# Kernel optimization log

Measured on AMD Instinct MI355X. Metric: run time of the kernel, lower is better.

## Reference

```python
import jax, jax.numpy as jnp
import numpy as np

B, Q, K, D, U = 8, 128, 512, 256, 256  # batch, q_len, kv_len, feat dim, units
NEG_INF = -1e6


def setup_inputs() -> dict:
    key = jax.random.key(0)
    ks = jax.random.split(key, 7)
    query = jax.random.normal(ks[0], (B, Q, D), dtype=jnp.float32)
    k_in = jax.random.normal(ks[1], (B, K, D), dtype=jnp.float32)
    value = jax.random.normal(ks[2], (B, K, D), dtype=jnp.float32)
    valid_len = jax.random.randint(ks[3], (B,), 1, K + 1, dtype=jnp.int32)
    s = 1.0 / np.sqrt(D)
    Wq = jax.random.uniform(ks[4], (D, U), jnp.float32, -s, s)
    Wk = jax.random.uniform(ks[5], (D, U), jnp.float32, -s, s)
    v_w = jax.random.uniform(ks[6], (U,), jnp.float32, -1.0 / np.sqrt(U), 1.0 / np.sqrt(U))
    return {"query": query, "key": k_in, "value": value, "valid_len": valid_len,
            "Wq": Wq, "Wk": Wk, "v_w": v_w}


def reference(query, key, value, valid_len, Wq, Wk, v_w):
    # projections: [B,Q,U] and [B,K,U]
    q = jnp.einsum('bqd,du->bqu', query, Wq)
    k = jnp.einsum('bkd,du->bku', key, Wk)
    # additive features [B,Q,K,U] -> tanh -> reduce with v: scores [B,Q,K]
    feats = jnp.tanh(q[:, :, None, :] + k[:, None, :, :])
    scores = jnp.einsum('bqku,u->bqk', feats, v_w)
    # masked softmax over keys: positions >= valid_len[b] masked out
    mask = jnp.arange(K)[None, None, :] < valid_len[:, None, None]
    scores = jnp.where(mask, scores, NEG_INF)
    attn = jax.nn.softmax(scores, axis=-1)
    # dropout p=0.0 (eval) -> identity
    return jnp.einsum('bqk,bkd->bqd', attn, value)
```

## Files before the change

### kernel.cpp

```cpp
#include <hip/hip_runtime.h>
#include <hip/hip_bf16.h>

#ifndef __has_builtin
#define __has_builtin(x) 0
#endif

__device__ __forceinline__ float fast_exp2(float x) {
#if __has_builtin(__builtin_amdgcn_exp2f)
  return __builtin_amdgcn_exp2f(x);
#else
  return exp2f(x);
#endif
}
__device__ __forceinline__ float fast_rcp(float x) {
#if __has_builtin(__builtin_amdgcn_rcpf)
  return __builtin_amdgcn_rcpf(x);
#else
  return 1.0f / x;
#endif
}

constexpr int Bsz = 8, QL = 128, KL = 512, DD = 256, UU = 256;
constexpr int PR = 4;
constexpr int DT = 8;
constexpr float NEG_INF = -1e6f;
constexpr float C2 = 2.885390081777927f;

__global__ __launch_bounds__(256) void proj_kernel(
    const float* __restrict__ query, const float* __restrict__ key,
    const float* __restrict__ Wq, const float* __restrict__ Wk,
    const int* __restrict__ valid_len,
    float* __restrict__ qp, float* __restrict__ kpT)
{
  const int u   = threadIdx.x;
  const int blk = blockIdx.x;

  constexpr int QBLKS = Bsz * QL / PR;
  const bool isQ = blk < QBLKS;
  const int  m0  = isQ ? blk * PR : (blk - QBLKS) * PR;

  const int kb_b = m0 / KL, kb_k0 = m0 % KL;
  if (!isQ) {
    if (kb_k0 >= valid_len[kb_b]) return;
  }
  const float* __restrict__ in = isQ ? query : key;
  const float* __restrict__ W  = isQ ? Wq : Wk;
  const float* r0 = in + (size_t)m0 * DD;

  float acc[PR];
#pragma unroll
  for (int r = 0; r < PR; ++r) acc[r] = 0.f;

  float  w_c[DT], w_n[DT];
  float4 r_c[PR][2], r_n[PR][2];

#pragma unroll
  for (int j = 0; j < DT; ++j) w_c[j] = W[j * UU + u];
#pragma unroll
  for (int r = 0; r < PR; ++r) {
    r_c[r][0] = *reinterpret_cast<const float4*>(r0 + r * DD);
    r_c[r][1] = *reinterpret_cast<const float4*>(r0 + r * DD + 4);
  }

  for (int d = 0; d < DD; d += DT) {
    const int dn = (d + DT < DD) ? d + DT : 0;
#pragma unroll
    for (int j = 0; j < DT; ++j) w_n[j] = W[(dn + j) * UU + u];
#pragma unroll
    for (int r = 0; r < PR; ++r) {
      r_n[r][0] = *reinterpret_cast<const float4*>(r0 + r * DD + dn);
      r_n[r][1] = *reinterpret_cast<const float4*>(r0 + r * DD + dn + 4);
    }
#pragma unroll
    for (int r = 0; r < PR; ++r) {
      float a = acc[r];
      a = fmaf(r_c[r][0].x, w_c[0], a);
      a = fmaf(r_c[r][0].y, w_c[1], a);
      a = fmaf(r_c[r][0].z, w_c[2], a);
      a = fmaf(r_c[r][0].w, w_c[3], a);
      a = fmaf(r_c[r][1].x, w_c[4], a);
      a = fmaf(r_c[r][1].y, w_c[5], a);
      a = fmaf(r_c[r][1].z, w_c[6], a);
      a = fmaf(r_c[r][1].w, w_c[7], a);
      acc[r] = a;
    }
#pragma unroll
    for (int j = 0; j < DT; ++j) w_c[j] = w_n[j];
#pragma unroll
    for (int r = 0; r < PR; ++r) { r_c[r][0] = r_n[r][0]; r_c[r][1] = r_n[r][1]; }
  }

  if (isQ) {
    float* o = qp + (size_t)m0 * UU + u;
#pragma unroll
    for (int r = 0; r < PR; ++r) o[(size_t)r * UU] = fast_exp2(acc[r] * C2);
  } else {
    float4 cv;
    cv.x = fast_exp2(acc[0] * C2); cv.y = fast_exp2(acc[1] * C2);
    cv.z = fast_exp2(acc[2] * C2); cv.w = fast_exp2(acc[3] * C2);
    *reinterpret_cast<float4*>(kpT + ((size_t)kb_b * UU + u) * KL + kb_k0) = cv;
  }
}

__global__ __launch_bounds__(512) void fused_attn_kernel(
    const float* __restrict__ value, const int* __restrict__ valid_len,
    const float* __restrict__ v_w, const float* __restrict__ qp,
    const float* __restrict__ kpT, float* __restrict__ out)
{
  __shared__ __align__(16) float4 qpack[UU];
  __shared__ __align__(16) float2 sp_part[8][8][64];
  __shared__ __align__(16) float  sps0[KL];
  __shared__ __align__(16) float  sps1[KL];
  __shared__ __align__(16) float2 opart[DD];
  __shared__ float2 redM[8], redS[8];

  const int t = threadIdx.x;
  const int w = t >> 6, l = t & 63;

  const int g = blockIdx.x;
  const int x = g & 7;
  const int i = g >> 3;
  int vl[8];
#pragma unroll
  for (int bi = 0; bi < 8; ++bi) vl[bi] = valid_len[bi];
  const int rk = (i < 32) ? x : (7 - x);
  int b = 0;
#pragma unroll
  for (int bi = 0; bi < 8; ++bi) {
    int r = 0;
#pragma unroll
    for (int bj = 0; bj < 8; ++bj)
      r += (vl[bj] > vl[bi]) || (vl[bj] == vl[bi] && bj < bi);
    if (r == rk) b = bi;
  }
  const int vlen = vl[b];
  const int q0 = i * 2;
  const int nc = (vlen + 63) >> 6;

  if (t < UU) {
    qpack[t] = make_float4(qp[(size_t)(b * QL + q0) * UU + t],
                           qp[(size_t)(b * QL + q0 + 1) * UU + t],
                           v_w[t], 0.f);
  }
  __syncthreads();

  {
    const float* __restrict__ kbase =
        kpT + ((size_t)(b * UU) + 32 * w) * KL + l;
    for (int c = 0; c < nc; ++c) {
      const int k64 = 64 * c;
      float a0 = 0.f, a1 = 0.f;
      float cb[8], nb[8];
#pragma unroll
      for (int j = 0; j < 8; ++j) cb[j] = kbase[(size_t)j * KL + k64];
#pragma unroll 1
      for (int ug = 0; ug < 32; ug += 8) {
        const int un = (ug + 8 < 32) ? ug + 8 : 0;
#pragma unroll
        for (int j = 0; j < 8; ++j) nb[j] = kbase[(size_t)(un + j) * KL + k64];
#pragma unroll
        for (int j = 0; j < 8; ++j) {
          const float4 qv = qpack[32 * w + ug + j];
          const float d0 = fmaf(qv.x, cb[j], 1.0f);
          const float d1 = fmaf(qv.y, cb[j], 1.0f);
          a0 = fmaf(qv.z, fast_rcp(d0), a0);
          a1 = fmaf(qv.z, fast_rcp(d1), a1);
        }
#pragma unroll
        for (int j = 0; j < 8; ++j) cb[j] = nb[j];
      }
      sp_part[w][c][l] = make_float2(a0, a1);
    }
  }
  __syncthreads();

  float s0 = 0.f, s1 = 0.f;
#pragma unroll
  for (int ws = 0; ws < 8; ++ws) {
    const float2 p = sp_part[ws][w][l];
    s0 += p.x; s1 += p.y;
  }
  const int key = t;
  s0 = (key < vlen) ? -(s0 + s0) : NEG_INF;
  s1 = (key < vlen) ? -(s1 + s1) : NEG_INF;

  float mx0 = s0, mx1 = s1;
#pragma unroll
  for (int off = 32; off >= 1; off >>= 1) {
    mx0 = fmaxf(mx0, __shfl_xor(mx0, off, 64));
    mx1 = fmaxf(mx1, __shfl_xor(mx1, off, 64));
  }
  if (l == 0) redM[w] = make_float2(mx0, mx1);
  __syncthreads();
  float m0 = redM[0].x, m1 = redM[0].y;
#pragma unroll
  for (int j = 1; j < 8; ++j) {
    m0 = fmaxf(m0, redM[j].x);
    m1 = fmaxf(m1, redM[j].y);
  }

  const float e0 = __expf(s0 - m0);
  const float e1 = __expf(s1 - m1);
  sps0[key] = e0;
  sps1[key] = e1;
  float ss0 = e0, ss1 = e1;
#pragma unroll
  for (int off = 32; off >= 1; off >>= 1) {
    ss0 += __shfl_xor(ss0, off, 64);
    ss1 += __shfl_xor(ss1, off, 64);
  }
  if (l == 0) redS[w] = make_float2(ss0, ss1);
  __syncthreads();
  float sum0 = redS[0].x, sum1 = redS[0].y;
#pragma unroll
  for (int j = 1; j < 8; ++j) {
    sum0 += redS[j].x;
    sum1 += redS[j].y;
  }
  const float inv0 = fast_rcp(sum0);
  const float inv1 = fast_rcp(sum1);

  const int h = t >> 8, d = t & 255;
  const int kmax  = (vlen + 15) & ~15;
  const int khalf = ((kmax >> 1) + 15) & ~15;
  const int kst = h ? khalf : 0;
  const int ken = h ? kmax : khalf;

  float o0 = 0.f, o1 = 0.f;
  if (ken > kst) {
    const float* __restrict__ vb = value + (size_t)b * KL * DD + d;
    float vc[16], vn[16];
#pragma unroll
    for (int j = 0; j < 16; ++j) vc[j] = vb[(size_t)(kst + j) * DD];
#pragma unroll 1
    for (int k = kst; k < ken; k += 16) {
      const int kn = (k + 16 < ken) ? k + 16 : kst;
#pragma unroll
      for (int j = 0; j < 16; ++j) vn[j] = vb[(size_t)(kn + j) * DD];
      const float4* __restrict__ p4 = reinterpret_cast<const float4*>(sps0 + k);
      const float4* __restrict__ q4 = reinterpret_cast<const float4*>(sps1 + k);
      const float4 p0 = p4[0], p1 = p4[1], p2 = p4[2], p3 = p4[3];
      const float4 r0 = q4[0], r1 = q4[1], r2 = q4[2], r3 = q4[3];
      o0 = fmaf(p0.x, vc[0],  o0); o1 = fmaf(r0.x, vc[0],  o1);
      o0 = fmaf(p0.y, vc[1],  o0); o1 = fmaf(r0.y, vc[1],  o1);
      o0 = fmaf(p0.z, vc[2],  o0); o1 = fmaf(r0.z, vc[2],  o1);
      o0 = fmaf(p0.w, vc[3],  o0); o1 = fmaf(r0.w, vc[3],  o1);
      o0 = fmaf(p1.x, vc[4],  o0); o1 = fmaf(r1.x, vc[4],  o1);
      o0 = fmaf(p1.y, vc[5],  o0); o1 = fmaf(r1.y, vc[5],  o1);
      o0 = fmaf(p1.z, vc[6],  o0); o1 = fmaf(r1.z, vc[6],  o1);
      o0 = fmaf(p1.w, vc[7],  o0); o1 = fmaf(r1.w, vc[7],  o1);
      o0 = fmaf(p2.x, vc[8],  o0); o1 = fmaf(r2.x, vc[8],  o1);
      o0 = fmaf(p2.y, vc[9],  o0); o1 = fmaf(r2.y, vc[9],  o1);
      o0 = fmaf(p2.z, vc[10], o0); o1 = fmaf(r2.z, vc[10], o1);
      o0 = fmaf(p2.w, vc[11], o0); o1 = fmaf(r2.w, vc[11], o1);
      o0 = fmaf(p3.x, vc[12], o0); o1 = fmaf(r3.x, vc[12], o1);
      o0 = fmaf(p3.y, vc[13], o0); o1 = fmaf(r3.y, vc[13], o1);
      o0 = fmaf(p3.z, vc[14], o0); o1 = fmaf(r3.z, vc[14], o1);
      o0 = fmaf(p3.w, vc[15], o0); o1 = fmaf(r3.w, vc[15], o1);
#pragma unroll
      for (int j = 0; j < 16; ++j) vc[j] = vn[j];
    }
  }
  if (h) opart[d] = make_float2(o0, o1);
  __syncthreads();
  if (!h) {
    const float2 p = opart[d];
    out[(size_t)(b * QL + q0) * DD + d]     = (o0 + p.x) * inv0;
    out[(size_t)(b * QL + q0 + 1) * DD + d] = (o1 + p.y) * inv1;
  }
}

extern "C" void kernel_launch(void* const* d_in, const int* in_sizes, int n_in,
                              void* d_out, int out_size, void* d_ws, size_t ws_size,
                              hipStream_t stream) {
  const float* query     = (const float*)d_in[0];
  const float* key       = (const float*)d_in[1];
  const float* value     = (const float*)d_in[2];
  const int*   valid_len = (const int*)d_in[3];
  const float* Wq        = (const float*)d_in[4];
  const float* Wk        = (const float*)d_in[5];
  const float* v_w       = (const float*)d_in[6];
  float* out = (float*)d_out;

  float* qp  = (float*)d_ws;
  float* kpT = qp + (size_t)Bsz * QL * UU;

  const int proj_blocks = (Bsz * QL + Bsz * KL) / PR;
  proj_kernel<<<proj_blocks, 256, 0, stream>>>(query, key, Wq, Wk, valid_len,
                                               qp, kpT);

  const int fused_blocks = Bsz * QL / 2;
  fused_attn_kernel<<<fused_blocks, 512, 0, stream>>>(value, valid_len, v_w,
                                                      qp, kpT, out);
}
```

Before: 113.3 us.

## Tile projection GEMM with shared-memory input rows and 8-row register blocking

The projection kernel now stages a 16-row input tile in shared memory and has each thread compute 8 rows for one of 128 output units, with two unit-halves per row tile. Each weight value loaded from global memory is reused across 8 rows instead of 4, which cuts redundant weight reads. Input rows are read from LDS as broadcasts instead of per-thread global loads. In exchange, the grid has fewer blocks, each carries a 16 KB LDS tile, and the loop is longer per thread. Masked key tiles are still skipped, but now at 16-row granularity.

```diff
diff --git a/kernel.cpp b/kernel.cpp
--- a/kernel.cpp
+++ b/kernel.cpp
@@ -21,10 +21,13 @@
 }
 
 constexpr int Bsz = 8, QL = 128, KL = 512, DD = 256, UU = 256;
-constexpr int PR = 4;
-constexpr int DT = 8;
 constexpr float NEG_INF = -1e6f;
 constexpr float C2 = 2.885390081777927f;
+
+constexpr int TR = 16;
+constexpr int TU = 128;
+constexpr int QTILES = (Bsz * QL / TR) * 2;
+constexpr int KTILES = (Bsz * KL / TR) * 2;
 
 __global__ __launch_bounds__(256) void proj_kernel(
     const float* __restrict__ query, const float* __restrict__ key,
@@ -32,73 +35,97 @@
     const int* __restrict__ valid_len,
     float* __restrict__ qp, float* __restrict__ kpT)
 {
-  const int u   = threadIdx.x;
+  __shared__ __align__(16) float As[TR][DD];
+
+  const int t   = threadIdx.x;
   const int blk = blockIdx.x;
-
-  constexpr int QBLKS = Bsz * QL / PR;
-  const bool isQ = blk < QBLKS;
-  const int  m0  = isQ ? blk * PR : (blk - QBLKS) * PR;
-
-  const int kb_b = m0 / KL, kb_k0 = m0 % KL;
+  const bool isQ = blk < QTILES;
+  const int  bb  = isQ ? blk : blk - QTILES;
+  const int  rt  = bb >> 1;
+  const int  ut  = bb & 1;
+  const int  r0  = rt * TR;
+
+  int kb_b = 0, kb_k0 = 0;
   if (!isQ) {
+    kb_b  = r0 >> 9;
+    kb_k0 = r0 & 511;
     if (kb_k0 >= valid_len[kb_b]) return;
   }
-  const float* __restrict__ in = isQ ? query : key;
-  const float* __restrict__ W  = isQ ? Wq : Wk;
-  const float* r0 = in + (size_t)m0 * DD;
-
-  float acc[PR];
-#pragma unroll
-  for (int r = 0; r < PR; ++r) acc[r] = 0.f;
-
-  float  w_c[DT], w_n[DT];
-  float4 r_c[PR][2], r_n[PR][2];
-
-#pragma unroll
-  for (int j = 0; j < DT; ++j) w_c[j] = W[j * UU + u];
-#pragma unroll
-  for (int r = 0; r < PR; ++r) {
-    r_c[r][0] = *reinterpret_cast<const float4*>(r0 + r * DD);
-    r_c[r][1] = *reinterpret_cast<const float4*>(r0 + r * DD + 4);
-  }
-
-  for (int d = 0; d < DD; d += DT) {
-    const int dn = (d + DT < DD) ? d + DT : 0;
-#pragma unroll
-    for (int j = 0; j < DT; ++j) w_n[j] = W[(dn + j) * UU + u];
-#pragma unroll
-    for (int r = 0; r < PR; ++r) {
-      r_n[r][0] = *reinterpret_cast<const float4*>(r0 + r * DD + dn);
-      r_n[r][1] = *reinterpret_cast<const float4*>(r0 + r * DD + dn + 4);
-    }
-#pragma unroll
-    for (int r = 0; r < PR; ++r) {
+
+  const int ul = t & 127;
+  const int rg = t >> 7;
+  const int u  = ut * TU + ul;
+
+  {
+    const float* __restrict__ src = (isQ ? query : key) + (size_t)r0 * DD;
+    const float4* __restrict__ s4 = reinterpret_cast<const float4*>(src);
+    float4* __restrict__ a4 = reinterpret_cast<float4*>(&As[0][0]);
+#pragma unroll
+    for (int i = 0; i < TR * DD / 4 / 256; ++i)
+      a4[t + 256 * i] = s4[t + 256 * i];
+  }
+  __syncthreads();
+
+  const float* __restrict__ W = (isQ ? Wq : Wk) + u;
+
+  float acc[8];
+#pragma unroll
+  for (int r = 0; r < 8; ++r) acc[r] = 0.f;
+
+  float wa[8], wb[8];
+#pragma unroll
+  for (int j = 0; j < 8; ++j) wa[j] = W[(size_t)j * UU];
+
+  const int rbase = rg * 8;
+
+  for (int dt = 0; dt < 32; dt += 2) {
+#pragma unroll
+    for (int j = 0; j < 8; ++j) wb[j] = W[(size_t)((dt + 1) * 8 + j) * UU];
+#pragma unroll
+    for (int r = 0; r < 8; ++r) {
+      const float* __restrict__ ar = &As[rbase + r][dt * 8];
+      const float4 x0 = *reinterpret_cast<const float4*>(ar);
+      const float4 x1 = *reinterpret_cast<const float4*>(ar + 4);
       float a = acc[r];
-      a = fmaf(r_c[r][0].x, w_c[0], a);
-      a = fmaf(r_c[r][0].y, w_c[1], a);
-      a = fmaf(r_c[r][0].z, w_c[2], a);
-      a = fmaf(r_c[r][0].w, w_c[3], a);
-      a = fmaf(r_c[r][1].x, w_c[4], a);
-      a = fmaf(r_c[r][1].y, w_c[5], a);
-      a = fmaf(r_c[r][1].z, w_c[6], a);
-      a = fmaf(r_c[r][1].w, w_c[7], a);
+      a = fmaf(x0.x, wa[0], a); a = fmaf(x0.y, wa[1], a);
+      a = fmaf(x0.z, wa[2], a); a = fmaf(x0.w, wa[3], a);
+      a = fmaf(x1.x, wa[4], a); a = fmaf(x1.y, wa[5], a);
+      a = fmaf(x1.z, wa[6], a); a = fmaf(x1.w, wa[7], a);
       acc[r] = a;
     }
-#pragma unroll
-    for (int j = 0; j < DT; ++j) w_c[j] = w_n[j];
-#pragma unroll
-    for (int r = 0; r < PR; ++r) { r_c[r][0] = r_n[r][0]; r_c[r][1] = r_n[r][1]; }
+    const int dne = (dt + 2 < 32) ? dt + 2 : 0;
+#pragma unroll
+    for (int j = 0; j < 8; ++j) wa[j] = W[(size_t)(dne * 8 + j) * UU];
+#pragma unroll
+    for (int r = 0; r < 8; ++r) {
+      const float* __restrict__ ar = &As[rbase + r][(dt + 1) * 8];
+      const float4 x0 = *reinterpret_cast<const float4*>(ar);
+      const float4 x1 = *reinterpret_cast<const float4*>(ar + 4);
+      float a = acc[r];
+      a = fmaf(x0.x, wb[0], a); a = fmaf(x0.y, wb[1], a);
+      a = fmaf(x0.z, wb[2], a); a = fmaf(x0.w, wb[3], a);
+      a = fmaf(x1.x, wb[4], a); a = fmaf(x1.y, wb[5], a);
+      a = fmaf(x1.z, wb[6], a); a = fmaf(x1.w, wb[7], a);
+      acc[r] = a;
+    }
   }
 
   if (isQ) {
-    float* o = qp + (size_t)m0 * UU + u;
-#pragma unroll
-    for (int r = 0; r < PR; ++r) o[(size_t)r * UU] = fast_exp2(acc[r] * C2);
+    const int qrow = r0 + rbase;
+    float* __restrict__ o = qp + (size_t)qrow * UU + u;
+#pragma unroll
+    for (int r = 0; r < 8; ++r)
+      o[(size_t)r * UU] = fast_exp2(acc[r] * C2);
   } else {
-    float4 cv;
-    cv.x = fast_exp2(acc[0] * C2); cv.y = fast_exp2(acc[1] * C2);
-    cv.z = fast_exp2(acc[2] * C2); cv.w = fast_exp2(acc[3] * C2);
-    *reinterpret_cast<float4*>(kpT + ((size_t)kb_b * UU + u) * KL + kb_k0) = cv;
+    const int k0 = kb_k0 + rbase;
+    float4 v0, v1;
+    v0.x = fast_exp2(acc[0] * C2); v0.y = fast_exp2(acc[1] * C2);
+    v0.z = fast_exp2(acc[2] * C2); v0.w = fast_exp2(acc[3] * C2);
+    v1.x = fast_exp2(acc[4] * C2); v1.y = fast_exp2(acc[5] * C2);
+    v1.z = fast_exp2(acc[6] * C2); v1.w = fast_exp2(acc[7] * C2);
+    float* __restrict__ dst = kpT + ((size_t)(kb_b * UU) + u) * KL + k0;
+    *reinterpret_cast<float4*>(dst)     = v0;
+    *reinterpret_cast<float4*>(dst + 4) = v1;
   }
 }
 
@@ -285,7 +312,7 @@
   float* qp  = (float*)d_ws;
   float* kpT = qp + (size_t)Bsz * QL * UU;
 
-  const int proj_blocks = (Bsz * QL + Bsz * KL) / PR;
+  const int proj_blocks = QTILES + KTILES;
   proj_kernel<<<proj_blocks, 256, 0, stream>>>(query, key, Wq, Wk, valid_len,
                                                qp, kpT);
 
```

Result: slower. 119.9 us (+5.8%).

## Compute projections with split-bf16 MFMA using pre-packed weight fragments

Applied to the files above, without the earlier changes.

Replaces the scalar FP32 FMA projection kernel with an MFMA kernel that splits each FP32 operand into hi and lo bf16 parts and accumulates three products, which keeps accuracy close to FP32. A new kernel packs Wq and Wk into MFMA fragment layout in a device global buffer on every call. The goal is to move the projection GEMMs onto matrix cores and make the weight loads contiguous. In exchange it adds an extra kernel launch and conversion work, and the three-term split drops the lo×lo term, so results are slightly less exact than the FP32 path.

```diff
diff --git a/kernel.cpp b/kernel.cpp
--- a/kernel.cpp
+++ b/kernel.cpp
@@ -21,84 +21,117 @@
 }
 
 constexpr int Bsz = 8, QL = 128, KL = 512, DD = 256, UU = 256;
-constexpr int PR = 4;
-constexpr int DT = 8;
 constexpr float NEG_INF = -1e6f;
 constexpr float C2 = 2.885390081777927f;
 
-__global__ __launch_bounds__(256) void proj_kernel(
+typedef __attribute__((ext_vector_type(8))) short bf16x8;
+typedef __attribute__((ext_vector_type(4))) float f32x4;
+
+__device__ __forceinline__ ushort f2bf(float x) {
+  uint u = __float_as_uint(x);
+  u += 0x7FFFu + ((u >> 16) & 1u);
+  return (ushort)(u >> 16);
+}
+__device__ __forceinline__ float bf2f(ushort h) {
+  return __uint_as_float(((uint)h) << 16);
+}
+
+__device__ ushort g_wpk[2][2][16][8][64][8];
+
+__global__ __launch_bounds__(256) void wpack_kernel(
+    const float* __restrict__ Wq, const float* __restrict__ Wk)
+{
+  const int tid = blockIdx.x * 256 + threadIdx.x;
+  const int src = tid >> 13;
+  const int ut  = (tid >> 9) & 15;
+  const int ks  = (tid >> 6) & 7;
+  const int l   = tid & 63;
+  const int u   = ut * 16 + (l & 15);
+  const int d0  = ks * 32 + (l >> 4) * 8;
+  const float* __restrict__ W = src ? Wk : Wq;
+
+  ushort hi[8], lo[8];
+#pragma unroll
+  for (int j = 0; j < 8; ++j) {
+    const float x = W[(size_t)(d0 + j) * UU + u];
+    const ushort h = f2bf(x);
+    hi[j] = h;
+    lo[j] = f2bf(x - bf2f(h));
+  }
+#pragma unroll
+  for (int j = 0; j < 8; ++j) g_wpk[src][0][ut][ks][l][j] = hi[j];
+#pragma unroll
+  for (int j = 0; j < 8; ++j) g_wpk[src][1][ut][ks][l][j] = lo[j];
+}
+
+__global__ __launch_bounds__(256) void proj_mfma_kernel(
     const float* __restrict__ query, const float* __restrict__ key,
-    const float* __restrict__ Wq, const float* __restrict__ Wk,
     const int* __restrict__ valid_len,
     float* __restrict__ qp, float* __restrict__ kpT)
 {
-  const int u   = threadIdx.x;
+  const int t = threadIdx.x, w = t >> 6, l = t & 63;
   const int blk = blockIdx.x;
-
-  constexpr int QBLKS = Bsz * QL / PR;
-  const bool isQ = blk < QBLKS;
-  const int  m0  = isQ ? blk * PR : (blk - QBLKS) * PR;
-
-  const int kb_b = m0 / KL, kb_k0 = m0 % KL;
-  if (!isQ) {
-    if (kb_k0 >= valid_len[kb_b]) return;
+  const bool isQ = blk < 64;
+
+  int b = 0, k0 = 0, row_mem;
+  if (isQ) {
+    row_mem = blk * 16;
+  } else {
+    const int kt = blk - 64;
+    b  = kt >> 5;
+    k0 = (kt & 31) * 16;
+    if (k0 >= valid_len[b]) return;
+    row_mem = b * KL + k0;
   }
   const float* __restrict__ in = isQ ? query : key;
-  const float* __restrict__ W  = isQ ? Wq : Wk;
-  const float* r0 = in + (size_t)m0 * DD;
-
-  float acc[PR];
-#pragma unroll
-  for (int r = 0; r < PR; ++r) acc[r] = 0.f;
-
-  float  w_c[DT], w_n[DT];
-  float4 r_c[PR][2], r_n[PR][2];
-
-#pragma unroll
-  for (int j = 0; j < DT; ++j) w_c[j] = W[j * UU + u];
-#pragma unroll
-  for (int r = 0; r < PR; ++r) {
-    r_c[r][0] = *reinterpret_cast<const float4*>(r0 + r * DD);
-    r_c[r][1] = *reinterpret_cast<const float4*>(r0 + r * DD + 4);
-  }
-
-  for (int d = 0; d < DD; d += DT) {
-    const int dn = (d + DT < DD) ? d + DT : 0;
-#pragma unroll
-    for (int j = 0; j < DT; ++j) w_n[j] = W[(dn + j) * UU + u];
-#pragma unroll
-    for (int r = 0; r < PR; ++r) {
-      r_n[r][0] = *reinterpret_cast<const float4*>(r0 + r * DD + dn);
-      r_n[r][1] = *reinterpret_cast<const float4*>(r0 + r * DD + dn + 4);
-    }
-#pragma unroll
-    for (int r = 0; r < PR; ++r) {
-      float a = acc[r];
-      a = fmaf(r_c[r][0].x, w_c[0], a);
-      a = fmaf(r_c[r][0].y, w_c[1], a);
-      a = fmaf(r_c[r][0].z, w_c[2], a);
-      a = fmaf(r_c[r][0].w, w_c[3], a);
-      a = fmaf(r_c[r][1].x, w_c[4], a);
-      a = fmaf(r_c[r][1].y, w_c[5], a);
-      a = fmaf(r_c[r][1].z, w_c[6], a);
-      a = fmaf(r_c[r][1].w, w_c[7], a);
-      acc[r] = a;
-    }
-#pragma unroll
-    for (int j = 0; j < DT; ++j) w_c[j] = w_n[j];
-#pragma unroll
-    for (int r = 0; r < PR; ++r) { r_c[r][0] = r_n[r][0]; r_c[r][1] = r_n[r][1]; }
-  }
-
-  if (isQ) {
-    float* o = qp + (size_t)m0 * UU + u;
-#pragma unroll
-    for (int r = 0; r < PR; ++r) o[(size_t)r * UU] = fast_exp2(acc[r] * C2);
-  } else {
-    float4 cv;
-    cv.x = fast_exp2(acc[0] * C2); cv.y = fast_exp2(acc[1] * C2);
-    cv.z = fast_exp2(acc[2] * C2); cv.w = fast_exp2(acc[3] * C2);
-    *reinterpret_cast<float4*>(kpT + ((size_t)kb_b * UU + u) * KL + kb_k0) = cv;
+  const int src = isQ ? 0 : 1;
+
+  bf16x8 Ah[8], Al[8];
+  {
+    const float* __restrict__ arow =
+        in + (size_t)(row_mem + (l & 15)) * DD + ((l >> 4) * 8);
+#pragma unroll
+    for (int s = 0; s < 8; ++s) {
+      const float4 x0 = *reinterpret_cast<const float4*>(arow + s * 32);
+      const float4 x1 = *reinterpret_cast<const float4*>(arow + s * 32 + 4);
+      const float v[8] = {x0.x, x0.y, x0.z, x0.w, x1.x, x1.y, x1.z, x1.w};
+#pragma unroll
+      for (int j = 0; j < 8; ++j) {
+        const ushort h = f2bf(v[j]);
+        Ah[s][j] = (short)h;
+        Al[s][j] = (short)f2bf(v[j] - bf2f(h));
+      }
+    }
+  }
+
+  const int ut0 = w * 4;
+#pragma unroll
+  for (int tt = 0; tt < 4; ++tt) {
+    const int ut = ut0 + tt;
+    f32x4 acc = {0.f, 0.f, 0.f, 0.f};
+#pragma unroll
+    for (int s = 0; s < 8; ++s) {
+      const bf16x8 bh = *reinterpret_cast<const bf16x8*>(&g_wpk[src][0][ut][s][l][0]);
+      const bf16x8 bl = *reinterpret_cast<const bf16x8*>(&g_wpk[src][1][ut][s][l][0]);
+      acc = __builtin_amdgcn_mfma_f32_16x16x32_bf16(Ah[s], bh, acc, 0, 0, 0);
+      acc = __builtin_amdgcn_mfma_f32_16x16x32_bf16(Al[s], bh, acc, 0, 0, 0);
+      acc = __builtin_amdgcn_mfma_f32_16x16x32_bf16(Ah[s], bl, acc, 0, 0, 0);
+    }
+    const int u  = ut * 16 + (l & 15);
+    const int r4 = (l >> 4) * 4;
+    if (isQ) {
+      float* __restrict__ o = qp + (size_t)(row_mem + r4) * UU + u;
+      o[0]          = fast_exp2(C2 * acc[0]);
+      o[UU]         = fast_exp2(C2 * acc[1]);
+      o[2 * UU]     = fast_exp2(C2 * acc[2]);
+      o[3 * UU]     = fast_exp2(C2 * acc[3]);
+    } else {
+      float4 v;
+      v.x = fast_exp2(C2 * acc[0]); v.y = fast_exp2(C2 * acc[1]);
+      v.z = fast_exp2(C2 * acc[2]); v.w = fast_exp2(C2 * acc[3]);
+      *reinterpret_cast<float4*>(
+          kpT + ((size_t)(b * UU) + u) * KL + k0 + r4) = v;
+    }
   }
 }
 
@@ -285,9 +318,11 @@
   float* qp  = (float*)d_ws;
   float* kpT = qp + (size_t)Bsz * QL * UU;
 
-  const int proj_blocks = (Bsz * QL + Bsz * KL) / PR;
-  proj_kernel<<<proj_blocks, 256, 0, stream>>>(query, key, Wq, Wk, valid_len,
-                                               qp, kpT);
+  wpack_kernel<<<64, 256, 0, stream>>>(Wq, Wk);
+
+  const int proj_blocks = 64 + 256;
+  proj_mfma_kernel<<<proj_blocks, 256, 0, stream>>>(query, key, valid_len,
+                                                    qp, kpT);
 
   const int fused_blocks = Bsz * QL / 2;
   fused_attn_kernel<<<fused_blocks, 512, 0, stream>>>(value, valid_len, v_w,
```

After: 108.1 us. 1.05x faster.
